# Performance work log

Hardware: AMD Instinct MI355X
Metric: run time of the kernel (lower is better)

Reference implementation:

```python
import jax, jax.numpy as jnp
import numpy as np

N_LAYERS = 8
N_MODELS = 9  # 1 big + 8 lil
F = 512
SPLIT = 16384
N_LIL = 2048  # rows per lil model; lil rows total = (N_MODELS-1)*N_LIL = 16384


def setup_inputs() -> dict:
    key = jax.random.key(0)
    k_x, k_wb, k_bb, k_wl, k_bl = jax.random.split(key, 5)
    scale = 1.0 / np.sqrt(F)  # keep activations stable across 8 layers
    x = jax.random.normal(k_x, (SPLIT + (N_MODELS - 1) * N_LIL, F), dtype=jnp.float32)
    Wbig = jax.random.normal(k_wb, (N_LAYERS, F, F), dtype=jnp.float32) * scale
    Bbig = jax.random.normal(k_bb, (N_LAYERS, F), dtype=jnp.float32) * 0.01
    Wlil = jax.random.normal(k_wl, (N_LAYERS, N_MODELS - 1, F, F), dtype=jnp.float32) * scale
    Blil = jax.random.normal(k_bl, (N_LAYERS, N_MODELS - 1, F), dtype=jnp.float32) * 0.01
    return {"x": x, "Wbig": Wbig, "Bbig": Bbig, "Wlil": Wlil, "Blil": Blil,
            "split": SPLIT, "n_lil": N_LIL}


def reference(x, Wbig, Bbig, Wlil, Blil, split, n_lil):
    n_layers, f = Wbig.shape[0], x.shape[1]
    n_lil_models = Wlil.shape[1]

    # Big stream: addmm(B, y, W) == y @ W + B, per layer.
    ybig = x[:split]
    for l in range(n_layers):
        ybig = ybig @ Wbig[l] + Bbig[l]

    # Lil stream: rows are grouped in blocks of n_lil per lil model
    # (repeat_interleave semantics). baddbmm(B[...,None], W, y[...,None])
    # computes (W @ y) + B per row => y @ W[m].T within model m.
    ylil = x[split:].reshape(n_lil_models, n_lil, f)  # [m, n, f]
    for l in range(n_layers):
        ylil = jnp.einsum('mnf,mgf->mng', ylil, Wlil[l]) + Blil[l][:, None, :]

    return jnp.concatenate([ybig, ylil.reshape(-1, f)], axis=0)
```

## Files before the change

kernel.cpp:

```cpp
#include <hip/hip_runtime.h>

typedef __bf16 bf16_t;
typedef bf16_t bf16x8 __attribute__((ext_vector_type(8)));
typedef bf16_t bf16x4 __attribute__((ext_vector_type(4)));
typedef float f32x4 __attribute__((ext_vector_type(4)));

#define F 512
#define NLAYERS 8
#define NLIL 8
#define TM 128
#define LSTR 520

__global__ void transpose_wbig(const float* __restrict__ W, bf16_t* __restrict__ out) {
  __shared__ float tile[64][65];
  const int l = blockIdx.z;
  const int tf = blockIdx.x, tg = blockIdx.y;
  const float* Wl = W + (size_t)l * F * F;
  bf16_t* Ol = out + (size_t)l * F * F;
  const int tx = threadIdx.x & 63;
  const int ty = threadIdx.x >> 6;
#pragma unroll
  for (int i = 0; i < 16; ++i) {
    int f = i * 4 + ty;
    tile[f][tx] = Wl[(size_t)(tf * 64 + f) * F + tg * 64 + tx];
  }
  __syncthreads();
#pragma unroll
  for (int i = 0; i < 16; ++i) {
    int g = i * 4 + ty;
    Ol[(size_t)(tg * 64 + g) * F + tf * 64 + tx] = (bf16_t)tile[tx][g];
  }
}

__global__ void convert_w(const float4* __restrict__ in, bf16x4* __restrict__ out, int n4) {
  int stride = gridDim.x * blockDim.x;
  for (int i = blockIdx.x * blockDim.x + threadIdx.x; i < n4; i += stride) {
    float4 v = in[i];
    bf16x4 o;
    o[0] = (bf16_t)v.x; o[1] = (bf16_t)v.y; o[2] = (bf16_t)v.z; o[3] = (bf16_t)v.w;
    out[i] = o;
  }
}

template <bool PREP>
__global__ __launch_bounds__(512, 2) void fused_mlp(
    const float* __restrict__ x,
    const bf16_t* __restrict__ WbigT, const bf16_t* __restrict__ WlilT,
    const float* __restrict__ WbigF, const float* __restrict__ WlilF,
    const float* __restrict__ Bbig, const float* __restrict__ Blil,
    float* __restrict__ out) {
  __shared__ alignas(16) bf16_t Y[TM * LSTR];

  const int tid = threadIdx.x;
  const int lane = tid & 63;
  const int wave = tid >> 6;
  const int ln15 = lane & 15;
  const int kq = (lane >> 4) << 3;
  const int rq = (lane >> 4) << 2;
  const int col0 = wave * 64;

  const int bid = blockIdx.x;
  const int xcd = bid & 7;
  const int slot = bid >> 3;
  int model, rb;
  if (slot < 16) { model = 1 + xcd; rb = slot; }
  else           { model = 0; rb = (xcd << 4) + (slot - 16); }

  const size_t grow = (model == 0) ? (size_t)rb * TM
                                   : (size_t)(16384 + (model - 1) * 2048 + rb * TM);

  {
    const float4* xs = (const float4*)(x + grow * F);
#pragma unroll
    for (int i = 0; i < 32; ++i) {
      int f4 = tid + i * 512;
      int row = f4 >> 7;
      int c4 = f4 & 127;
      float4 v = xs[f4];
      bf16x4 o;
      o[0] = (bf16_t)v.x; o[1] = (bf16_t)v.y; o[2] = (bf16_t)v.z; o[3] = (bf16_t)v.w;
      *(bf16x4*)&Y[row * LSTR + c4 * 4] = o;
    }
  }
  __syncthreads();

  for (int l = 0; l < NLAYERS; ++l) {
    const bf16_t* Wt = nullptr;
    const float* Wf = nullptr;
    if (PREP)
      Wt = (model == 0) ? WbigT + (size_t)l * F * F
                        : WlilT + (size_t)(l * NLIL + (model - 1)) * F * F;
    else
      Wf = (model == 0) ? WbigF + (size_t)l * F * F
                        : WlilF + (size_t)(l * NLIL + (model - 1)) * F * F;
    const float* Bp = (model == 0) ? Bbig + (size_t)l * F
                                   : Blil + (size_t)(l * NLIL + (model - 1)) * F;

    f32x4 acc[8][4];
#pragma unroll
    for (int ni = 0; ni < 4; ++ni) {
      float bv = Bp[col0 + ni * 16 + ln15];
      f32x4 bi = {bv, bv, bv, bv};
#pragma unroll
      for (int mi = 0; mi < 8; ++mi) acc[mi][ni] = bi;
    }

#pragma unroll 2
    for (int ks = 0; ks < 16; ++ks) {
      const int kk = ks * 32 + kq;
      bf16x8 a[8];
#pragma unroll
      for (int mi = 0; mi < 8; ++mi)
        a[mi] = *(const bf16x8*)&Y[(mi * 16 + ln15) * LSTR + kk];
      bf16x8 b[4];
      if (PREP) {
#pragma unroll
        for (int ni = 0; ni < 4; ++ni)
          b[ni] = *(const bf16x8*)&Wt[(size_t)(col0 + ni * 16 + ln15) * F + kk];
      } else if (model != 0) {
#pragma unroll
        for (int ni = 0; ni < 4; ++ni) {
          const float* p = Wf + (size_t)(col0 + ni * 16 + ln15) * F + kk;
          float4 u = *(const float4*)p;
          float4 v = *(const float4*)(p + 4);
          bf16x8 t;
          t[0] = (bf16_t)u.x; t[1] = (bf16_t)u.y; t[2] = (bf16_t)u.z; t[3] = (bf16_t)u.w;
          t[4] = (bf16_t)v.x; t[5] = (bf16_t)v.y; t[6] = (bf16_t)v.z; t[7] = (bf16_t)v.w;
          b[ni] = t;
        }
      } else {
#pragma unroll
        for (int ni = 0; ni < 4; ++ni) {
          int col = col0 + ni * 16 + ln15;
          bf16x8 t;
#pragma unroll
          for (int j = 0; j < 8; ++j) t[j] = (bf16_t)Wf[(size_t)(kk + j) * F + col];
          b[ni] = t;
        }
      }
#pragma unroll
      for (int mi = 0; mi < 8; ++mi)
#pragma unroll
        for (int ni = 0; ni < 4; ++ni)
          acc[mi][ni] = __builtin_amdgcn_mfma_f32_16x16x32_bf16(a[mi], b[ni], acc[mi][ni], 0, 0, 0);
    }
    __syncthreads();

    if (l < NLAYERS - 1) {
#pragma unroll
      for (int mi = 0; mi < 8; ++mi)
#pragma unroll
        for (int ni = 0; ni < 4; ++ni) {
          int row = mi * 16 + rq;
          int col = col0 + ni * 16 + ln15;
#pragma unroll
          for (int r = 0; r < 4; ++r)
            Y[(row + r) * LSTR + col] = (bf16_t)acc[mi][ni][r];
        }
      __syncthreads();
    } else {
      float* op = out + grow * F;
#pragma unroll
      for (int mi = 0; mi < 8; ++mi)
#pragma unroll
        for (int ni = 0; ni < 4; ++ni) {
          int row = mi * 16 + rq;
          int col = col0 + ni * 16 + ln15;
#pragma unroll
          for (int r = 0; r < 4; ++r)
            op[(size_t)(row + r) * F + col] = acc[mi][ni][r];
        }
    }
  }
}

extern "C" void kernel_launch(void* const* d_in, const int* in_sizes, int n_in,
                              void* d_out, int out_size, void* d_ws, size_t ws_size,
                              hipStream_t stream) {
  const float* x    = (const float*)d_in[0];
  const float* Wbig = (const float*)d_in[1];
  const float* Bbig = (const float*)d_in[2];
  const float* Wlil = (const float*)d_in[3];
  const float* Blil = (const float*)d_in[4];
  float* out = (float*)d_out;

  const size_t nWbig = (size_t)NLAYERS * F * F;
  const size_t nWlil = (size_t)NLAYERS * NLIL * F * F;
  const size_t need = (nWbig + nWlil) * sizeof(bf16_t);

  if (ws_size >= need) {
    bf16_t* WbigT = (bf16_t*)d_ws;
    bf16_t* WlilB = WbigT + nWbig;
    transpose_wbig<<<dim3(8, 8, NLAYERS), 256, 0, stream>>>(Wbig, WbigT);
    convert_w<<<4096, 256, 0, stream>>>((const float4*)Wlil, (bf16x4*)WlilB,
                                        (int)(nWlil / 4));
    fused_mlp<true><<<256, 512, 0, stream>>>(x, WbigT, WlilB, nullptr, nullptr,
                                             Bbig, Blil, out);
  } else {
    fused_mlp<false><<<256, 512, 0, stream>>>(x, nullptr, nullptr, Wbig, Wlil,
                                              Bbig, Blil, out);
  }
}
```

Baseline: 341.0 us.

## Swap MFMA operand roles, use 1024-thread blocks and XOR-swizzled LDS

The fused MLP kernel now puts the weights in the MFMA A operand and the activations in the B operand, which computes the transposed product. Each of 16 waves now covers 32 output columns across all 128 rows. The padded LDS row stride is replaced by an XOR swizzle, so layer outputs are written back as packed bf16x4 and the final outputs are stored as float4 vectors. This aims to raise occupancy, cut per-wave weight traffic and avoid LDS bank conflicts. In exchange each wave reads all activation rows from LDS every k-step, and the 1024-thread launch bound tightens register limits.

```diff
diff --git a/kernel.cpp b/kernel.cpp
--- a/kernel.cpp
+++ b/kernel.cpp
@@ -9,7 +9,6 @@
 #define NLAYERS 8
 #define NLIL 8
 #define TM 128
-#define LSTR 520
 
 __global__ void transpose_wbig(const float* __restrict__ W, bf16_t* __restrict__ out) {
   __shared__ float tile[64][65];
@@ -42,22 +41,27 @@
   }
 }
 
+__device__ __forceinline__ int ysw(int m, int k) {
+  return m * F + ((((k >> 3) ^ (m & 7)) << 3) | (k & 7));
+}
+
 template <bool PREP>
-__global__ __launch_bounds__(512, 2) void fused_mlp(
+__global__ __launch_bounds__(1024, 4) void fused_mlp(
     const float* __restrict__ x,
     const bf16_t* __restrict__ WbigT, const bf16_t* __restrict__ WlilT,
     const float* __restrict__ WbigF, const float* __restrict__ WlilF,
     const float* __restrict__ Bbig, const float* __restrict__ Blil,
     float* __restrict__ out) {
-  __shared__ alignas(16) bf16_t Y[TM * LSTR];
+  __shared__ alignas(16) bf16_t Y[TM * F];
 
   const int tid = threadIdx.x;
   const int lane = tid & 63;
   const int wave = tid >> 6;
   const int ln15 = lane & 15;
-  const int kq = (lane >> 4) << 3;
-  const int rq = (lane >> 4) << 2;
-  const int col0 = wave * 64;
+  const int q = lane >> 4;
+  const int kq = q << 3;
+  const int rq = q << 2;
+  const int g0 = wave * 32;
 
   const int bid = blockIdx.x;
   const int xcd = bid & 7;
@@ -72,14 +76,14 @@
   {
     const float4* xs = (const float4*)(x + grow * F);
 #pragma unroll
-    for (int i = 0; i < 32; ++i) {
-      int f4 = tid + i * 512;
+    for (int i = 0; i < 16; ++i) {
+      int f4 = tid + i * 1024;
       int row = f4 >> 7;
       int c4 = f4 & 127;
       float4 v = xs[f4];
       bf16x4 o;
       o[0] = (bf16_t)v.x; o[1] = (bf16_t)v.y; o[2] = (bf16_t)v.z; o[3] = (bf16_t)v.w;
-      *(bf16x4*)&Y[row * LSTR + c4 * 4] = o;
+      *(bf16x4*)&Y[ysw(row, c4 * 4)] = o;
     }
   }
   __syncthreads();
@@ -96,79 +100,78 @@
     const float* Bp = (model == 0) ? Bbig + (size_t)l * F
                                    : Blil + (size_t)(l * NLIL + (model - 1)) * F;
 
-    f32x4 acc[8][4];
-#pragma unroll
-    for (int ni = 0; ni < 4; ++ni) {
-      float bv = Bp[col0 + ni * 16 + ln15];
-      f32x4 bi = {bv, bv, bv, bv};
-#pragma unroll
-      for (int mi = 0; mi < 8; ++mi) acc[mi][ni] = bi;
+    f32x4 acc[2][8];
+#pragma unroll
+    for (int gi = 0; gi < 2; ++gi) {
+      f32x4 bi = *(const f32x4*)&Bp[g0 + gi * 16 + rq];
+#pragma unroll
+      for (int mi = 0; mi < 8; ++mi) acc[gi][mi] = bi;
     }
 
 #pragma unroll 2
     for (int ks = 0; ks < 16; ++ks) {
       const int kk = ks * 32 + kq;
-      bf16x8 a[8];
-#pragma unroll
-      for (int mi = 0; mi < 8; ++mi)
-        a[mi] = *(const bf16x8*)&Y[(mi * 16 + ln15) * LSTR + kk];
-      bf16x8 b[4];
+      bf16x8 aW[2];
       if (PREP) {
 #pragma unroll
-        for (int ni = 0; ni < 4; ++ni)
-          b[ni] = *(const bf16x8*)&Wt[(size_t)(col0 + ni * 16 + ln15) * F + kk];
+        for (int gi = 0; gi < 2; ++gi)
+          aW[gi] = *(const bf16x8*)&Wt[(size_t)(g0 + gi * 16 + ln15) * F + kk];
       } else if (model != 0) {
 #pragma unroll
-        for (int ni = 0; ni < 4; ++ni) {
-          const float* p = Wf + (size_t)(col0 + ni * 16 + ln15) * F + kk;
+        for (int gi = 0; gi < 2; ++gi) {
+          const float* p = Wf + (size_t)(g0 + gi * 16 + ln15) * F + kk;
           float4 u = *(const float4*)p;
           float4 v = *(const float4*)(p + 4);
           bf16x8 t;
           t[0] = (bf16_t)u.x; t[1] = (bf16_t)u.y; t[2] = (bf16_t)u.z; t[3] = (bf16_t)u.w;
           t[4] = (bf16_t)v.x; t[5] = (bf16_t)v.y; t[6] = (bf16_t)v.z; t[7] = (bf16_t)v.w;
-          b[ni] = t;
+          aW[gi] = t;
         }
       } else {
 #pragma unroll
-        for (int ni = 0; ni < 4; ++ni) {
-          int col = col0 + ni * 16 + ln15;
+        for (int gi = 0; gi < 2; ++gi) {
+          int col = g0 + gi * 16 + ln15;
           bf16x8 t;
 #pragma unroll
           for (int j = 0; j < 8; ++j) t[j] = (bf16_t)Wf[(size_t)(kk + j) * F + col];
-          b[ni] = t;
+          aW[gi] = t;
         }
       }
+      bf16x8 bY[8];
+      const int chunk = (ks * 4 + q) ^ (ln15 & 7);
 #pragma unroll
       for (int mi = 0; mi < 8; ++mi)
-#pragma unroll
-        for (int ni = 0; ni < 4; ++ni)
-          acc[mi][ni] = __builtin_amdgcn_mfma_f32_16x16x32_bf16(a[mi], b[ni], acc[mi][ni], 0, 0, 0);
+        bY[mi] = *(const bf16x8*)&Y[(mi * 16 + ln15) * F + (chunk << 3)];
+#pragma unroll
+      for (int gi = 0; gi < 2; ++gi)
+#pragma unroll
+        for (int mi = 0; mi < 8; ++mi)
+          acc[gi][mi] = __builtin_amdgcn_mfma_f32_16x16x32_bf16(aW[gi], bY[mi], acc[gi][mi], 0, 0, 0);
     }
     __syncthreads();
 
     if (l < NLAYERS - 1) {
 #pragma unroll
-      for (int mi = 0; mi < 8; ++mi)
-#pragma unroll
-        for (int ni = 0; ni < 4; ++ni) {
-          int row = mi * 16 + rq;
-          int col = col0 + ni * 16 + ln15;
-#pragma unroll
-          for (int r = 0; r < 4; ++r)
-            Y[(row + r) * LSTR + col] = (bf16_t)acc[mi][ni][r];
+      for (int gi = 0; gi < 2; ++gi)
+#pragma unroll
+        for (int mi = 0; mi < 8; ++mi) {
+          int m = mi * 16 + ln15;
+          int g = g0 + gi * 16 + rq;
+          bf16x4 t;
+#pragma unroll
+          for (int r = 0; r < 4; ++r) t[r] = (bf16_t)acc[gi][mi][r];
+          *(bf16x4*)&Y[ysw(m, g)] = t;
         }
       __syncthreads();
     } else {
       float* op = out + grow * F;
 #pragma unroll
-      for (int mi = 0; mi < 8; ++mi)
-#pragma unroll
-        for (int ni = 0; ni < 4; ++ni) {
-          int row = mi * 16 + rq;
-          int col = col0 + ni * 16 + ln15;
-#pragma unroll
-          for (int r = 0; r < 4; ++r)
-            op[(size_t)(row + r) * F + col] = acc[mi][ni][r];
+      for (int gi = 0; gi < 2; ++gi)
+#pragma unroll
+        for (int mi = 0; mi < 8; ++mi) {
+          int m = mi * 16 + ln15;
+          int g = g0 + gi * 16 + rq;
+          *(f32x4*)&op[(size_t)m * F + g] = acc[gi][mi];
         }
     }
   }
@@ -194,10 +197,10 @@
     transpose_wbig<<<dim3(8, 8, NLAYERS), 256, 0, stream>>>(Wbig, WbigT);
     convert_w<<<4096, 256, 0, stream>>>((const float4*)Wlil, (bf16x4*)WlilB,
                                         (int)(nWlil / 4));
-    fused_mlp<true><<<256, 512, 0, stream>>>(x, WbigT, WlilB, nullptr, nullptr,
-                                             Bbig, Blil, out);
+    fused_mlp<true><<<256, 1024, 0, stream>>>(x, WbigT, WlilB, nullptr, nullptr,
+                                              Bbig, Blil, out);
   } else {
-    fused_mlp<false><<<256, 512, 0, stream>>>(x, nullptr, nullptr, Wbig, Wlil,
-                                              Bbig, Blil, out);
-  }
-}
+    fused_mlp<false><<<256, 1024, 0, stream>>>(x, nullptr, nullptr, Wbig, Wlil,
+                                               Bbig, Blil, out);
+  }
+}
```

After: 329.3 us. 3.5% less time.
